# Kernel optimization log

Hardware: AMD Instinct MI355X
Metric: run time of the kernel (lower is better)

## Reference

```python
import jax, jax.numpy as jnp
import numpy as np

RADIUS = 4


def setup_inputs() -> dict:
    key = jax.random.key(0)
    k1, k2, k3 = jax.random.split(key, 3)
    B, C, H, W = 1, 256, 64, 128  # 1/8-res features of a 512x1024 image
    fmap1 = jax.random.normal(k1, (B, C, H, W), dtype=jnp.float32)
    fmap2 = jax.random.normal(k2, (B, C, H, W), dtype=jnp.float32)
    # coords: pixel-space sampling centers, channel dim = (x, y)
    u = jax.random.uniform(k3, (B, 2, H, W), dtype=jnp.float32)
    scale = jnp.array([W - 1, H - 1], dtype=jnp.float32).reshape(1, 2, 1, 1)
    coords = u * scale
    return {"fmap1": fmap1, "fmap2": fmap2, "coords": coords}


def corr_lookup(fmap1, fmap2, coords, radius=RADIUS):
    """CorrBlock.__init__ + __call__: dense corr volume + 9x9 bilinear lookup."""
    B, C, H, W = fmap1.shape
    # full correlation volume [B, h, w, h2, w2], scaled by 1/sqrt(dim)
    corr = jnp.einsum('bchw,bcHW->bhwHW', fmap1, fmap2) / jnp.sqrt(jnp.float32(C))
    corrf = corr.reshape(B, H, W, H * W)

    r = radius
    K = 2 * r + 1
    dx = jnp.linspace(-r, r, K, dtype=jnp.float32)
    dy = jnp.linspace(-r, r, K, dtype=jnp.float32)
    delta = jnp.stack(jnp.meshgrid(dx, dy, indexing='ij'), axis=-1)  # [K,K,2] (x,y)

    c = jnp.transpose(coords, (0, 2, 3, 1))            # [B,H,W,2]
    pts = c[:, :, :, None, None, :] + delta            # [B,H,W,K,K,2]

    # normalize to [-1,1] then denormalize with align_corners=True (faithful to
    # torch grid_sample; identity here since grid and volume share H,W)
    gx = 2.0 * pts[..., 0] / (W - 1) - 1.0
    gy = 2.0 * pts[..., 1] / (H - 1) - 1.0
    x = (gx + 1.0) * 0.5 * (W - 1)
    y = (gy + 1.0) * 0.5 * (H - 1)

    x0 = jnp.floor(x)
    y0 = jnp.floor(y)
    wx1 = x - x0
    wy1 = y - y0
    wx0 = 1.0 - wx1
    wy0 = 1.0 - wy1

    def gather(yi, xi):
        # zero padding for out-of-bounds (grid_sample default padding_mode)
        valid = ((yi >= 0) & (yi < H) & (xi >= 0) & (xi < W)).astype(jnp.float32)
        yc = jnp.clip(yi, 0, H - 1).astype(jnp.int32)
        xc = jnp.clip(xi, 0, W - 1).astype(jnp.int32)
        idx = (yc * W + xc).reshape(B, H, W, K * K)
        v = jnp.take_along_axis(corrf, idx, axis=-1).reshape(B, H, W, K, K)
        return v * valid

    out = (gather(y0, x0) * wy0 * wx0
           + gather(y0, x0 + 1.0) * wy0 * wx1
           + gather(y0 + 1.0, x0) * wy1 * wx0
           + gather(y0 + 1.0, x0 + 1.0) * wy1 * wx1)  # [B,H,W,K,K]

    return jnp.transpose(out.reshape(B, H, W, K * K), (0, 3, 1, 2))  # [B,K*K,H,W]


def reference(fmap1, fmap2, coords):
    return corr_lookup(fmap1, fmap2, coords, RADIUS)
```

## Files before the change

kernel.cpp:

```cpp
#include <hip/hip_runtime.h>
#include <hip/hip_bf16.h>

#define HH 64
#define WW 128
#define HW 8192
#define CC 256

typedef unsigned uv4 __attribute__((ext_vector_type(4)));

__device__ __forceinline__ float bf_lo(unsigned u) { return __uint_as_float(u << 16); }
__device__ __forceinline__ float bf_hi(unsigned u) { return __uint_as_float(u & 0xffff0000u); }

__global__ __launch_bounds__(256) void transpose_both(
    const float* __restrict__ f1, const float* __restrict__ f2,
    __hip_bfloat16* __restrict__ f1T, __hip_bfloat16* __restrict__ f2T)
{
  const float* src = blockIdx.z ? f2 : f1;
  __hip_bfloat16* dst = blockIdx.z ? f2T : f1T;
  float scale = blockIdx.z ? 1.0f : 0.0625f;

  __shared__ float tile[32][33];
  int tx = threadIdx.x, ty = threadIdx.y;
  int pos0 = blockIdx.x * 32, c0 = blockIdx.y * 32;
#pragma unroll
  for (int r = 0; r < 4; ++r)
    tile[ty + r * 8][tx] =
        __builtin_nontemporal_load(&src[(size_t)(c0 + ty + r * 8) * HW + pos0 + tx]) * scale;
  __syncthreads();
#pragma unroll
  for (int r = 0; r < 4; ++r)
    dst[(size_t)(pos0 + ty + r * 8) * CC + c0 + tx] =
        __float2bfloat16(tile[tx][ty + r * 8]);
}

__global__ __launch_bounds__(256) void corr_main(
    const float* __restrict__ coords,
    const unsigned* __restrict__ f1T,
    const unsigned* __restrict__ f2T,
    float* __restrict__ out)
{
  int tid  = threadIdx.x;
  int wave = tid >> 6;
  int lane = tid & 63;
  int g    = lane >> 4;
  int q    = lane & 15;
  int p    = blockIdx.x * 4 + wave;

  float x = __builtin_nontemporal_load(&coords[p]);
  float y = __builtin_nontemporal_load(&coords[HW + p]);
  float x0f = floorf(x), y0f = floorf(y);
  float fx = x - x0f, fy = y - y0f;
  int ix0 = (int)x0f - 4;
  int iy0 = (int)y0f - 4;

  const uv4* f1p = (const uv4*)(f1T + (size_t)p * 128 + q * 8);
  uv4 A0 = __builtin_nontemporal_load(f1p);
  uv4 A1 = __builtin_nontemporal_load(f1p + 1);
  float f1v[16] = { bf_lo(A0.x), bf_hi(A0.x), bf_lo(A0.y), bf_hi(A0.y),
                    bf_lo(A0.z), bf_hi(A0.z), bf_lo(A0.w), bf_hi(A0.w),
                    bf_lo(A1.x), bf_hi(A1.x), bf_lo(A1.y), bf_hi(A1.y),
                    bf_lo(A1.z), bf_hi(A1.z), bf_lo(A1.w), bf_hi(A1.w) };

  __shared__ float dots[4][100];

#pragma unroll 2
  for (int t = 0; t < 25; ++t) {
    int n = t * 4 + g;
    int u = n / 10;
    int v = n - u * 10;
    int gx = ix0 + u, gy = iy0 + v;
    bool valid = (gx >= 0) && (gx < WW) && (gy >= 0) && (gy < HH);
    int pos = valid ? (gy * WW + gx) : 0;
    const uv4* f2p = (const uv4*)(f2T + (size_t)pos * 128 + q * 8);
    uv4 B0 = f2p[0], B1 = f2p[1];
    float acc =      bf_lo(B0.x) * f1v[0];
    acc = fmaf(bf_hi(B0.x), f1v[1],  acc);
    acc = fmaf(bf_lo(B0.y), f1v[2],  acc);
    acc = fmaf(bf_hi(B0.y), f1v[3],  acc);
    acc = fmaf(bf_lo(B0.z), f1v[4],  acc);
    acc = fmaf(bf_hi(B0.z), f1v[5],  acc);
    acc = fmaf(bf_lo(B0.w), f1v[6],  acc);
    acc = fmaf(bf_hi(B0.w), f1v[7],  acc);
    acc = fmaf(bf_lo(B1.x), f1v[8],  acc);
    acc = fmaf(bf_hi(B1.x), f1v[9],  acc);
    acc = fmaf(bf_lo(B1.y), f1v[10], acc);
    acc = fmaf(bf_hi(B1.y), f1v[11], acc);
    acc = fmaf(bf_lo(B1.z), f1v[12], acc);
    acc = fmaf(bf_hi(B1.z), f1v[13], acc);
    acc = fmaf(bf_lo(B1.w), f1v[14], acc);
    acc = fmaf(bf_hi(B1.w), f1v[15], acc);
    acc += __shfl_xor(acc, 1);
    acc += __shfl_xor(acc, 2);
    acc += __shfl_xor(acc, 4);
    acc += __shfl_xor(acc, 8);
    if (q == 0) dots[wave][n] = valid ? acc : 0.0f;
  }

  __syncthreads();

  float wx1 = fx, wx0 = 1.0f - fx, wy1 = fy, wy0 = 1.0f - fy;
  for (int k = lane; k < 81; k += 64) {
    int i = k / 9;
    int j = k - i * 9;
    float d00 = dots[wave][i * 10 + j];
    float d10 = dots[wave][(i + 1) * 10 + j];
    float d01 = dots[wave][i * 10 + j + 1];
    float d11 = dots[wave][(i + 1) * 10 + j + 1];
    float o = wy0 * fmaf(wx1, d10, wx0 * d00) + wy1 * fmaf(wx1, d11, wx0 * d01);
    __builtin_nontemporal_store(o, &out[(size_t)k * HW + p]);
  }
}

__global__ __launch_bounds__(64) void corr_fallback(
    const float* __restrict__ coords, const float* __restrict__ f1,
    const float* __restrict__ f2, float* __restrict__ out)
{
  int lane = threadIdx.x;
  int p = blockIdx.x;
  float x = coords[p], y = coords[HW + p];
  float x0f = floorf(x), y0f = floorf(y);
  float fx = x - x0f, fy = y - y0f;
  int ix0 = (int)x0f - 4, iy0 = (int)y0f - 4;
  float f1v[4];
#pragma unroll
  for (int k = 0; k < 4; ++k)
    f1v[k] = f1[(size_t)(lane + 64 * k) * HW + p] * 0.0625f;
  __shared__ float dots[100];
  for (int n = 0; n < 100; ++n) {
    int u = n / 10, v = n - u * 10;
    int gx = ix0 + u, gy = iy0 + v;
    bool valid = (gx >= 0) && (gx < WW) && (gy >= 0) && (gy < HH);
    int pos = valid ? (gy * WW + gx) : 0;
    float acc = 0.0f;
#pragma unroll
    for (int k = 0; k < 4; ++k)
      acc = fmaf(f1v[k], f2[(size_t)(lane + 64 * k) * HW + pos], acc);
    acc += __shfl_xor(acc, 1);
    acc += __shfl_xor(acc, 2);
    acc += __shfl_xor(acc, 4);
    acc += __shfl_xor(acc, 8);
    acc += __shfl_xor(acc, 16);
    acc += __shfl_xor(acc, 32);
    if (lane == 0) dots[n] = valid ? acc : 0.0f;
  }
  __syncthreads();
  float wx1 = fx, wx0 = 1.0f - fx, wy1 = fy, wy0 = 1.0f - fy;
  for (int k = lane; k < 81; k += 64) {
    int i = k / 9, j = k - i * 9;
    float d00 = dots[i * 10 + j];
    float d10 = dots[(i + 1) * 10 + j];
    float d01 = dots[i * 10 + j + 1];
    float d11 = dots[(i + 1) * 10 + j + 1];
    float o = wy0 * fmaf(wx1, d10, wx0 * d00) + wy1 * fmaf(wx1, d11, wx0 * d01);
    out[(size_t)k * HW + p] = o;
  }
}

extern "C" void kernel_launch(void* const* d_in, const int* in_sizes, int n_in,
                              void* d_out, int out_size, void* d_ws, size_t ws_size,
                              hipStream_t stream) {
  const float* fmap1  = (const float*)d_in[0];
  const float* fmap2  = (const float*)d_in[1];
  const float* coords = (const float*)d_in[2];
  float* out = (float*)d_out;

  size_t need = (size_t)HW * CC * sizeof(__hip_bfloat16) * 2;
  if (ws_size >= need) {
    __hip_bfloat16* f1T = (__hip_bfloat16*)d_ws;
    __hip_bfloat16* f2T = f1T + (size_t)HW * CC;
    dim3 tb(32, 8), tg(HW / 32, CC / 32, 2);
    hipLaunchKernelGGL(transpose_both, tg, tb, 0, stream, fmap1, fmap2, f1T, f2T);
    corr_main<<<dim3(HW / 4), dim3(256), 0, stream>>>(
        coords, (const unsigned*)f1T, (const unsigned*)f2T, out);
  } else {
    corr_fallback<<<dim3(HW), dim3(64), 0, stream>>>(coords, fmap1, fmap2, out);
  }
}
```

Before: 44.27 us.

## Quantize transposed features to per-row int8 and use sdot4 dot products

Adds a kernel that quantizes each bf16 feature row to int8 with a per-pixel absmax scale. The correlation kernel then computes dot products with packed int8 sdot4 instructions and rescales them. This halves the bytes gathered per neighbour and cuts ALU work. In exchange it adds an extra kernel launch and a full pass over the bf16 buffers, and it lowers numerical precision.

```diff
diff --git a/kernel.cpp b/kernel.cpp
--- a/kernel.cpp
+++ b/kernel.cpp
@@ -7,9 +7,23 @@
 #define CC 256
 
 typedef unsigned uv4 __attribute__((ext_vector_type(4)));
+typedef unsigned uv2 __attribute__((ext_vector_type(2)));
 
 __device__ __forceinline__ float bf_lo(unsigned u) { return __uint_as_float(u << 16); }
 __device__ __forceinline__ float bf_hi(unsigned u) { return __uint_as_float(u & 0xffff0000u); }
+
+__device__ __forceinline__ int dot4(unsigned a, unsigned b, int c) {
+#if __has_builtin(__builtin_amdgcn_sdot4)
+  return __builtin_amdgcn_sdot4((int)a, (int)b, c, false);
+#else
+  int r = c;
+  r += ((int)(a << 24) >> 24) * ((int)(b << 24) >> 24);
+  r += ((int)(a << 16) >> 24) * ((int)(b << 16) >> 24);
+  r += ((int)(a <<  8) >> 24) * ((int)(b <<  8) >> 24);
+  r += ((int)a >> 24)         * ((int)b >> 24);
+  return r;
+#endif
+}
 
 __global__ __launch_bounds__(256) void transpose_both(
     const float* __restrict__ f1, const float* __restrict__ f2,
@@ -33,10 +47,56 @@
         __float2bfloat16(tile[tx][ty + r * 8]);
 }
 
-__global__ __launch_bounds__(256) void corr_main(
+__global__ __launch_bounds__(256) void quant_rows(
+    const uv4* __restrict__ f1T, const uv4* __restrict__ f2T,
+    uv2* __restrict__ f1q, uv2* __restrict__ f2q,
+    float* __restrict__ s1, float* __restrict__ s2)
+{
+  const uv4* srcT = blockIdx.z ? f2T : f1T;
+  uv2* dq = blockIdx.z ? f2q : f1q;
+  float* ds = blockIdx.z ? s2 : s1;
+
+  int tid = threadIdx.x;
+  int w = tid >> 6, lane = tid & 63;
+  int h = lane & 31;
+  int pos = blockIdx.x * 8 + w * 2 + (lane >> 5);
+
+  uv4 B = __builtin_nontemporal_load(&srcT[(size_t)pos * 32 + h]);
+  float v[8] = { bf_lo(B.x), bf_hi(B.x), bf_lo(B.y), bf_hi(B.y),
+                 bf_lo(B.z), bf_hi(B.z), bf_lo(B.w), bf_hi(B.w) };
+  float m = fabsf(v[0]);
+#pragma unroll
+  for (int i = 1; i < 8; ++i) m = fmaxf(m, fabsf(v[i]));
+  m = fmaxf(m, __shfl_xor(m, 1));
+  m = fmaxf(m, __shfl_xor(m, 2));
+  m = fmaxf(m, __shfl_xor(m, 4));
+  m = fmaxf(m, __shfl_xor(m, 8));
+  m = fmaxf(m, __shfl_xor(m, 16));
+
+  float inv = (m > 0.0f) ? 127.0f / m : 0.0f;
+  if (h == 0) ds[pos] = m * (1.0f / 127.0f);
+
+  unsigned lo = 0, hi = 0;
+#pragma unroll
+  for (int i = 0; i < 4; ++i) {
+    int qi = (int)rintf(v[i] * inv);
+    lo |= ((unsigned)(qi & 0xff)) << (8 * i);
+  }
+#pragma unroll
+  for (int i = 0; i < 4; ++i) {
+    int qi = (int)rintf(v[4 + i] * inv);
+    hi |= ((unsigned)(qi & 0xff)) << (8 * i);
+  }
+  uv2 o; o.x = lo; o.y = hi;
+  dq[(size_t)pos * 32 + h] = o;
+}
+
+__global__ __launch_bounds__(256) void corr_int8(
     const float* __restrict__ coords,
-    const unsigned* __restrict__ f1T,
-    const unsigned* __restrict__ f2T,
+    const uv4* __restrict__ f1q,
+    const uv4* __restrict__ f2q,
+    const float* __restrict__ s1,
+    const float* __restrict__ s2,
     float* __restrict__ out)
 {
   int tid  = threadIdx.x;
@@ -53,17 +113,12 @@
   int ix0 = (int)x0f - 4;
   int iy0 = (int)y0f - 4;
 
-  const uv4* f1p = (const uv4*)(f1T + (size_t)p * 128 + q * 8);
-  uv4 A0 = __builtin_nontemporal_load(f1p);
-  uv4 A1 = __builtin_nontemporal_load(f1p + 1);
-  float f1v[16] = { bf_lo(A0.x), bf_hi(A0.x), bf_lo(A0.y), bf_hi(A0.y),
-                    bf_lo(A0.z), bf_hi(A0.z), bf_lo(A0.w), bf_hi(A0.w),
-                    bf_lo(A1.x), bf_hi(A1.x), bf_lo(A1.y), bf_hi(A1.y),
-                    bf_lo(A1.z), bf_hi(A1.z), bf_lo(A1.w), bf_hi(A1.w) };
+  float s1v = s1[p];
+  uv4 A = __builtin_nontemporal_load(&f1q[(size_t)p * 16 + q]);
 
   __shared__ float dots[4][100];
 
-#pragma unroll 2
+#pragma unroll 5
   for (int t = 0; t < 25; ++t) {
     int n = t * 4 + g;
     int u = n / 10;
@@ -71,29 +126,14 @@
     int gx = ix0 + u, gy = iy0 + v;
     bool valid = (gx >= 0) && (gx < WW) && (gy >= 0) && (gy < HH);
     int pos = valid ? (gy * WW + gx) : 0;
-    const uv4* f2p = (const uv4*)(f2T + (size_t)pos * 128 + q * 8);
-    uv4 B0 = f2p[0], B1 = f2p[1];
-    float acc =      bf_lo(B0.x) * f1v[0];
-    acc = fmaf(bf_hi(B0.x), f1v[1],  acc);
-    acc = fmaf(bf_lo(B0.y), f1v[2],  acc);
-    acc = fmaf(bf_hi(B0.y), f1v[3],  acc);
-    acc = fmaf(bf_lo(B0.z), f1v[4],  acc);
-    acc = fmaf(bf_hi(B0.z), f1v[5],  acc);
-    acc = fmaf(bf_lo(B0.w), f1v[6],  acc);
-    acc = fmaf(bf_hi(B0.w), f1v[7],  acc);
-    acc = fmaf(bf_lo(B1.x), f1v[8],  acc);
-    acc = fmaf(bf_hi(B1.x), f1v[9],  acc);
-    acc = fmaf(bf_lo(B1.y), f1v[10], acc);
-    acc = fmaf(bf_hi(B1.y), f1v[11], acc);
-    acc = fmaf(bf_lo(B1.z), f1v[12], acc);
-    acc = fmaf(bf_hi(B1.z), f1v[13], acc);
-    acc = fmaf(bf_lo(B1.w), f1v[14], acc);
-    acc = fmaf(bf_hi(B1.w), f1v[15], acc);
+    uv4 B = f2q[(size_t)pos * 16 + q];
+    float s2v = s2[pos];
+    int acc = dot4(A.x, B.x, dot4(A.y, B.y, dot4(A.z, B.z, dot4(A.w, B.w, 0))));
     acc += __shfl_xor(acc, 1);
     acc += __shfl_xor(acc, 2);
     acc += __shfl_xor(acc, 4);
     acc += __shfl_xor(acc, 8);
-    if (q == 0) dots[wave][n] = valid ? acc : 0.0f;
+    if (q == 0) dots[wave][n] = valid ? (float)acc * s1v * s2v : 0.0f;
   }
 
   __syncthreads();
@@ -164,14 +204,26 @@
   const float* coords = (const float*)d_in[2];
   float* out = (float*)d_out;
 
-  size_t need = (size_t)HW * CC * sizeof(__hip_bfloat16) * 2;
+  const size_t szT = (size_t)HW * CC * 2;
+  const size_t szQ = (size_t)HW * CC;
+  const size_t szS = (size_t)HW * 4;
+  const size_t need = 2 * szT + 2 * szQ + 2 * szS;
+
   if (ws_size >= need) {
-    __hip_bfloat16* f1T = (__hip_bfloat16*)d_ws;
-    __hip_bfloat16* f2T = f1T + (size_t)HW * CC;
+    char* w = (char*)d_ws;
+    __hip_bfloat16* f1T = (__hip_bfloat16*)w;
+    __hip_bfloat16* f2T = (__hip_bfloat16*)(w + szT);
+    unsigned char*  f1q = (unsigned char*)(w + 2 * szT);
+    unsigned char*  f2q = (unsigned char*)(w + 2 * szT + szQ);
+    float*          s1  = (float*)(w + 2 * szT + 2 * szQ);
+    float*          s2  = (float*)(w + 2 * szT + 2 * szQ + szS);
+
     dim3 tb(32, 8), tg(HW / 32, CC / 32, 2);
     hipLaunchKernelGGL(transpose_both, tg, tb, 0, stream, fmap1, fmap2, f1T, f2T);
-    corr_main<<<dim3(HW / 4), dim3(256), 0, stream>>>(
-        coords, (const unsigned*)f1T, (const unsigned*)f2T, out);
+    quant_rows<<<dim3(HW / 8, 1, 2), dim3(256), 0, stream>>>(
+        (const uv4*)f1T, (const uv4*)f2T, (uv2*)f1q, (uv2*)f2q, s1, s2);
+    corr_int8<<<dim3(HW / 4), dim3(256), 0, stream>>>(
+        coords, (const uv4*)f1q, (const uv4*)f2q, s1, s2, out);
   } else {
     corr_fallback<<<dim3(HW), dim3(64), 0, stream>>>(coords, fmap1, fmap2, out);
   }
```

New measurement: 43.14 us. -2.6%, faster.
